# Performance work log

Hardware: AMD Instinct MI355X
Metric: run time of the kernel (lower is better)

The kernel has to match this reference:

```python
import jax, jax.numpy as jnp
import numpy as np

D_MODEL = 1024
NUM_HEADS = 16
HEAD_DIM = D_MODEL // NUM_HEADS


def setup_inputs() -> dict:
    key = jax.random.key(0)
    ks = jax.random.split(key, 11)
    N, S = 4, 2048
    s = 1.0 / np.sqrt(D_MODEL)
    return {
        "query": jax.random.normal(ks[0], (N, S, D_MODEL), jnp.float32),
        "key": jax.random.normal(ks[1], (N, S, D_MODEL), jnp.float32),
        "value": jax.random.normal(ks[2], (N, S, D_MODEL), jnp.float32),
        "Wq": jax.random.normal(ks[3], (D_MODEL, D_MODEL), jnp.float32) * s,
        "bq": jnp.zeros((D_MODEL,), jnp.float32),
        "Wk": jax.random.normal(ks[4], (D_MODEL, D_MODEL), jnp.float32) * s,
        "bk": jnp.zeros((D_MODEL,), jnp.float32),
        "Wv": jax.random.normal(ks[5], (D_MODEL, D_MODEL), jnp.float32) * s,
        "bv": jnp.zeros((D_MODEL,), jnp.float32),
        "Wo": jax.random.normal(ks[6], (D_MODEL, D_MODEL), jnp.float32) * s,
        "bo": jnp.zeros((D_MODEL,), jnp.float32),
    }


def reference(query, key, value, Wq, bq, Wk, bk, Wv, bv, Wo, bo):
    N, Q, _ = query.shape
    K = key.shape[1]
    # torch Linear: x @ W^T + b
    q = (query @ Wq.T + bq).reshape(N, Q, NUM_HEADS, HEAD_DIM)
    k = (key @ Wk.T + bk).reshape(N, K, NUM_HEADS, HEAD_DIM)
    v = (value @ Wv.T + bv).reshape(N, K, NUM_HEADS, HEAD_DIM)
    # NOTE: original module applies NO 1/sqrt(head_dim) scaling.
    scores = jnp.einsum('nqhd,nkhd->nhqk', q, k)
    attn = jax.nn.softmax(scores, axis=3)
    out = jnp.einsum('nhqk,nkhd->nqhd', attn, v).reshape(N, Q, D_MODEL)
    return out @ Wo.T + bo
```

## Files before the change

### kernel.cpp

```cpp
#include <hip/hip_runtime.h>
#include <stdint.h>

#define SEQ 2048
#define MROWS 8192
#define LOG2E 1.44269504f

typedef __attribute__((ext_vector_type(8))) _Float16 f16x8;
typedef __attribute__((ext_vector_type(2))) __fp16 fp16x2_t;
typedef __attribute__((ext_vector_type(8))) unsigned short ushort8;
typedef __attribute__((ext_vector_type(4))) unsigned short ushort4_t;
typedef __attribute__((ext_vector_type(4))) float f32x4;

__device__ __forceinline__ unsigned short f32_to_f16u(float f) {
  union { _Float16 h; unsigned short u; } v; v.h = (_Float16)f; return v.u;
}

__device__ __forceinline__ ushort8 pack8_rtz(float4 f0, float4 f1) {
  union { fp16x2_t h2[4]; ushort8 u8; } pk;
  pk.h2[0] = __builtin_amdgcn_cvt_pkrtz(f0.x, f0.y);
  pk.h2[1] = __builtin_amdgcn_cvt_pkrtz(f0.z, f0.w);
  pk.h2[2] = __builtin_amdgcn_cvt_pkrtz(f1.x, f1.y);
  pk.h2[3] = __builtin_amdgcn_cvt_pkrtz(f1.z, f1.w);
  return pk.u8;
}

__device__ __forceinline__ void gload16(const void* g, void* l) {
  __builtin_amdgcn_global_load_lds(
      (const __attribute__((address_space(1))) unsigned int*)g,
      (__attribute__((address_space(3))) unsigned int*)l, 16, 0, 0);
}

__global__ __launch_bounds__(256) void wconv_k(
    const float* __restrict__ Wq, const float* __restrict__ Wk,
    const float* __restrict__ Wv, const float* __restrict__ Wo,
    unsigned short* __restrict__ WF)
{
  const int plane = blockIdx.y;
  const float* __restrict__ s = (plane==0)? Wq : (plane==1)? Wk : (plane==2)? Wv : Wo;
  size_t off = ((size_t)blockIdx.x*256 + threadIdx.x) * 8;
  float4 f0 = *(const float4*)(s + off);
  float4 f1 = *(const float4*)(s + off + 4);
  *(ushort8*)&WF[(size_t)plane*1048576 + off] = pack8_rtz(f0, f1);
}

__global__ __launch_bounds__(256) void qkv_k(
    const float* __restrict__ Aq, const float* __restrict__ Ak, const float* __restrict__ Av,
    const unsigned short* __restrict__ WF,
    const float* __restrict__ bq, const float* __restrict__ bk, const float* __restrict__ bv,
    unsigned short* __restrict__ Qf, unsigned short* __restrict__ Kf, unsigned short* __restrict__ Vt)
{
  const int z = blockIdx.z;
  const float* __restrict__ A    = (z==0)? Aq : (z==1)? Ak : Av;
  const unsigned short* __restrict__ W = WF + (size_t)z*1048576;
  const float* __restrict__ bias = (z==0)? bq : (z==1)? bk : bv;

  __shared__ unsigned short Ah[128*32];
  __shared__ unsigned short Bh[128*32];

  const int tid  = threadIdx.x;
  const int lane = tid & 63;
  const int w    = tid >> 6;
  const int wm   = w >> 1, wn = w & 1;
  const int row0 = blockIdx.x * 128;
  const int col0 = blockIdx.y * 128;

  f32x4 acc[4][4] = {};

  for (int k0 = 0; k0 < 1024; k0 += 32) {
    __syncthreads();
    #pragma unroll
    for (int j=0;j<2;++j) {
      int r  = w*32 + j*16 + (lane>>2);
      int sl = (lane & 3) ^ ((r>>1)&3);
      gload16(W + (size_t)(col0 + r)*1024 + k0 + sl*8, &Bh[(w*32 + j*16)*32]);
    }
    #pragma unroll
    for (int i = 0; i < 2; ++i) {
      int c = tid + i*256;
      int r = c >> 2, slot = c & 3;
      int lidx = r*32 + ((slot ^ ((r >> 1) & 3))*8);
      const float* ap = A + (size_t)(row0 + r)*1024 + k0 + slot*8;
      float4 f0 = *(const float4*)ap;
      float4 f1 = *(const float4*)(ap + 4);
      *(ushort8*)&Ah[lidx] = pack8_rtz(f0, f1);
    }
    __syncthreads();

    f16x8 a_[4], b_[4];
    const int slotR = lane >> 4;
    #pragma unroll
    for (int m=0;m<4;++m) {
      int r = wm*64 + m*16 + (lane & 15);
      a_[m] = *(const f16x8*)&Ah[r*32 + ((slotR ^ ((r>>1)&3))*8)];
    }
    #pragma unroll
    for (int nn=0;nn<4;++nn) {
      int r = wn*64 + nn*16 + (lane & 15);
      b_[nn] = *(const f16x8*)&Bh[r*32 + ((slotR ^ ((r>>1)&3))*8)];
    }
    #pragma unroll
    for (int m=0;m<4;++m)
      #pragma unroll
      for (int nn=0;nn<4;++nn)
        acc[m][nn] = __builtin_amdgcn_mfma_f32_16x16x32_f16(a_[m], b_[nn], acc[m][nn],0,0,0);
  }

  #pragma unroll
  for (int m=0;m<4;++m) {
    #pragma unroll
    for (int nn=0;nn<4;++nn) {
      int gcol = col0 + wn*64 + nn*16 + (lane & 15);
      float bsv = bias[gcol];
      if (z == 2) {
        int rbase = row0 + wm*64 + m*16 + (lane>>4)*4;
        int nIdx = rbase >> 11, s0 = rbase & 2047;
        ushort4_t pk;
        #pragma unroll
        for (int r2=0;r2<4;++r2) pk[r2] = f32_to_f16u(acc[m][nn][r2] + bsv);
        *(ushort4_t*)&Vt[((size_t)(nIdx*1024 + gcol))*2048 + s0] = pk;
      } else {
        unsigned short* __restrict__ dst = (z==0)? Qf : Kf;
        const float qsc = (z==0)? LOG2E : 1.0f;
        #pragma unroll
        for (int r2=0;r2<4;++r2) {
          int grow = row0 + wm*64 + m*16 + (lane>>4)*4 + r2;
          dst[(size_t)grow*1024 + gcol] = f32_to_f16u((acc[m][nn][r2] + bsv) * qsc);
        }
      }
    }
  }
}

__global__ __launch_bounds__(256) void oproj_k(
    const unsigned short* __restrict__ AO, const unsigned short* __restrict__ W,
    const float* __restrict__ bias, float* __restrict__ out)
{
  __shared__ unsigned short Ah[128*32];
  __shared__ unsigned short Bh[128*32];

  const int tid  = threadIdx.x;
  const int lane = tid & 63;
  const int w    = tid >> 6;
  const int wm   = w >> 1, wn = w & 1;
  const int row0 = blockIdx.x * 128;
  const int col0 = blockIdx.y * 128;

  f32x4 acc[4][4] = {};

  for (int k0 = 0; k0 < 1024; k0 += 32) {
    __syncthreads();
    #pragma unroll
    for (int j=0;j<2;++j) {
      int r  = w*32 + j*16 + (lane>>2);
      int sl = (lane & 3) ^ ((r>>1)&3);
      gload16(AO + (size_t)(row0 + r)*1024 + k0 + sl*8, &Ah[(w*32 + j*16)*32]);
      gload16(W  + (size_t)(col0 + r)*1024 + k0 + sl*8, &Bh[(w*32 + j*16)*32]);
    }
    __syncthreads();

    f16x8 a_[4], b_[4];
    const int slotR = lane >> 4;
    #pragma unroll
    for (int m=0;m<4;++m) {
      int r = wm*64 + m*16 + (lane & 15);
      a_[m] = *(const f16x8*)&Ah[r*32 + ((slotR ^ ((r>>1)&3))*8)];
    }
    #pragma unroll
    for (int nn=0;nn<4;++nn) {
      int r = wn*64 + nn*16 + (lane & 15);
      b_[nn] = *(const f16x8*)&Bh[r*32 + ((slotR ^ ((r>>1)&3))*8)];
    }
    #pragma unroll
    for (int m=0;m<4;++m)
      #pragma unroll
      for (int nn=0;nn<4;++nn)
        acc[m][nn] = __builtin_amdgcn_mfma_f32_16x16x32_f16(a_[m], b_[nn], acc[m][nn],0,0,0);
  }

  #pragma unroll
  for (int m=0;m<4;++m)
    #pragma unroll
    for (int nn=0;nn<4;++nn) {
      int gcol = col0 + wn*64 + nn*16 + (lane & 15);
      float bsv = bias[gcol];
      #pragma unroll
      for (int r2=0;r2<4;++r2) {
        int grow = row0 + wm*64 + m*16 + (lane>>4)*4 + r2;
        out[(size_t)grow*1024 + gcol] = acc[m][nn][r2] + bsv;
      }
    }
}

__global__ __launch_bounds__(256) void attn_k(
  const unsigned short* __restrict__ Qf, const unsigned short* __restrict__ Kf,
  const unsigned short* __restrict__ Vt, unsigned short* __restrict__ AO)
{
  __shared__ unsigned short Ks[2][64*64];
  __shared__ unsigned short Vs[2][64*64];
  __shared__ unsigned short Ps[4][32*64];

  const int tid = threadIdx.x, lane = tid & 63, w = tid >> 6;
  const int q = lane & 15, g = lane >> 4;

  const int bid = blockIdx.x;
  const int swz = (bid & 7) * 128 + (bid >> 3);
  const int qt = swz & 15, nh = swz >> 4;
  const int n = nh >> 4, h = nh & 15;

  f16x8 qf[2][2];
  #pragma unroll
  for (int qm=0; qm<2; ++qm) {
    int qrow = n*SEQ + qt*128 + w*32 + qm*16 + q;
    #pragma unroll
    for (int ks=0; ks<2; ++ks)
      qf[qm][ks] = *(const f16x8*)&Qf[(size_t)qrow*1024 + h*64 + ks*32 + g*8];
  }

  f32x4 o[2][4] = {};
  float mrun[2] = {-1e30f,-1e30f}, lrun[2] = {0.f,0.f};

  const size_t kbase = (size_t)(n*SEQ)*1024 + h*64;
  const size_t vbase = ((size_t)(n*1024 + h*64))*SEQ;

  #pragma unroll
  for (int i=0;i<2;++i){
    int c = tid + i*256; int r = c>>3, sl = c&7;
    int lidx = r*64 + ((sl^(r&7))*8);
    *(ushort8*)&Ks[0][lidx] = *(const ushort8*)&Kf[kbase + (size_t)r*1024 + sl*8];
    *(ushort8*)&Vs[0][lidx] = *(const ushort8*)&Vt[vbase + (size_t)r*SEQ + sl*8];
  }
  __syncthreads();

  int cur = 0;
  for (int kt = 0; kt < 32; ++kt) {
    f32x4 s[2][4];
    #pragma unroll
    for (int qm=0;qm<2;++qm)
      #pragma unroll
      for (int nf=0; nf<4; ++nf) s[qm][nf] = f32x4{0.f,0.f,0.f,0.f};
    __builtin_amdgcn_s_setprio(1);
    #pragma unroll
    for (int nf=0; nf<4; ++nf) {
      int rr = nf*16 + q;
      #pragma unroll
      for (int ks=0; ks<2; ++ks) {
        f16x8 kb = *(const f16x8*)&Ks[cur][rr*64 + (((ks*4+g)^(q&7))*8)];
        s[0][nf] = __builtin_amdgcn_mfma_f32_16x16x32_f16(kb, qf[0][ks], s[0][nf],0,0,0);
        s[1][nf] = __builtin_amdgcn_mfma_f32_16x16x32_f16(kb, qf[1][ks], s[1][nf],0,0,0);
      }
    }
    __builtin_amdgcn_s_setprio(0);

    ushort8 kreg[2], vreg[2];
    if (kt < 31) {
      #pragma unroll
      for (int i=0;i<2;++i){
        int c = tid + i*256; int r = c>>3, sl = c&7;
        kreg[i] = *(const ushort8*)&Kf[kbase + (size_t)((kt+1)*64 + r)*1024 + sl*8];
        vreg[i] = *(const ushort8*)&Vt[vbase + (size_t)r*SEQ + (kt+1)*64 + sl*8];
      }
    }

    #pragma unroll
    for (int qm=0; qm<2; ++qm) {
      float ml = fmaxf(fmaxf(fmaxf(s[qm][0][0],s[qm][0][1]),fmaxf(s[qm][0][2],s[qm][0][3])),
                       fmaxf(fmaxf(s[qm][1][0],s[qm][1][1]),fmaxf(s[qm][1][2],s[qm][1][3])));
      float mh = fmaxf(fmaxf(fmaxf(s[qm][2][0],s[qm][2][1]),fmaxf(s[qm][2][2],s[qm][2][3])),
                       fmaxf(fmaxf(s[qm][3][0],s[qm][3][1]),fmaxf(s[qm][3][2],s[qm][3][3])));
      ml = fmaxf(ml, mh);
      if (!__all(ml <= mrun[qm] + 7.0f)) {
        float m1 = fmaxf(ml, __shfl_xor(ml, 16, 64));
        float m2 = fmaxf(m1, __shfl_xor(m1, 32, 64));
        float mn = fmaxf(mrun[qm], m2);
        float sc = __builtin_amdgcn_exp2f(mrun[qm] - mn);
        lrun[qm] *= sc;
        mrun[qm] = mn;
        #pragma unroll
        for (int df=0; df<4; ++df)
          #pragma unroll
          for (int r=0;r<4;++r) o[qm][df][r] *= sc;
      }
      float m0 = mrun[qm];
      float pvv[16]; float rsl = 0.f;
      #pragma unroll
      for (int nf=0; nf<4; ++nf)
        #pragma unroll
        for (int r=0;r<4;++r) {
          float p = __builtin_amdgcn_exp2f(s[qm][nf][r] - m0);
          pvv[nf*4+r] = p; rsl += p;
        }
      lrun[qm] += rsl;

      #pragma unroll
      for (int nf=0; nf<4; ++nf) {
        union { fp16x2_t h2[2]; ushort4_t u4; } pk;
        pk.h2[0] = __builtin_amdgcn_cvt_pkrtz(pvv[nf*4+0], pvv[nf*4+1]);
        pk.h2[1] = __builtin_amdgcn_cvt_pkrtz(pvv[nf*4+2], pvv[nf*4+3]);
        int gi = 2*nf + (g>>1);
        int idx = (qm*16+q)*64 + ((gi ^ (q&7))*8) + (g&1)*4;
        *(ushort4_t*)&Ps[w][idx] = pk.u4;
      }
    }

    #pragma unroll
    for (int s2=0; s2<2; ++s2) {
      int sl = 4*s2 + g;
      f16x8 pa0 = *(const f16x8*)&Ps[w][(q    )*64 + ((sl^(q&7))*8)];
      f16x8 pa1 = *(const f16x8*)&Ps[w][(16+q)*64 + ((sl^(q&7))*8)];
      __builtin_amdgcn_s_setprio(1);
      #pragma unroll
      for (int df=0; df<4; ++df) {
        f16x8 vb = *(const f16x8*)&Vs[cur][(df*16+q)*64 + ((sl^(q&7))*8)];
        o[0][df] = __builtin_amdgcn_mfma_f32_16x16x32_f16(vb, pa0, o[0][df],0,0,0);
        o[1][df] = __builtin_amdgcn_mfma_f32_16x16x32_f16(vb, pa1, o[1][df],0,0,0);
      }
      __builtin_amdgcn_s_setprio(0);
    }

    if (kt < 31) {
      #pragma unroll
      for (int i=0;i<2;++i){
        int c = tid + i*256; int r = c>>3, sl = c&7;
        int lidx = r*64 + ((sl^(r&7))*8);
        *(ushort8*)&Ks[cur^1][lidx] = kreg[i];
        *(ushort8*)&Vs[cur^1][lidx] = vreg[i];
      }
    }
    __syncthreads();
    cur ^= 1;
  }

  #pragma unroll
  for (int qm=0; qm<2; ++qm) {
    float rs = lrun[qm];
    rs += __shfl_xor(rs, 16, 64);
    rs += __shfl_xor(rs, 32, 64);
    float inv = 1.0f / rs;
    int qrow = n*SEQ + qt*128 + w*32 + qm*16 + q;
    #pragma unroll
    for (int df=0; df<4; ++df)
      #pragma unroll
      for (int r=0;r<4;++r)
        AO[(size_t)qrow*1024 + h*64 + df*16 + g*4 + r] = f32_to_f16u(o[qm][df][r] * inv);
  }
}

extern "C" void kernel_launch(void* const* d_in, const int* in_sizes, int n_in,
                              void* d_out, int out_size, void* d_ws, size_t ws_size,
                              hipStream_t stream)
{
  (void)in_sizes; (void)n_in; (void)out_size; (void)ws_size;
  const float* query = (const float*)d_in[0];
  const float* key   = (const float*)d_in[1];
  const float* value = (const float*)d_in[2];
  const float* Wq = (const float*)d_in[3];
  const float* bq = (const float*)d_in[4];
  const float* Wk = (const float*)d_in[5];
  const float* bk = (const float*)d_in[6];
  const float* Wv = (const float*)d_in[7];
  const float* bv = (const float*)d_in[8];
  const float* Wo = (const float*)d_in[9];
  const float* bo = (const float*)d_in[10];
  float* out = (float*)d_out;

  unsigned short* ws = (unsigned short*)d_ws;
  const size_t PLANE = (size_t)MROWS * 1024;
  unsigned short* Qf = ws;
  unsigned short* Kf = Qf + PLANE;
  unsigned short* Vt = Kf + PLANE;
  unsigned short* AO = Vt + PLANE;
  unsigned short* WF = AO + PLANE;

  dim3 bb(256);
  wconv_k<<<dim3(512,4), bb, 0, stream>>>(Wq, Wk, Wv, Wo, WF);
  qkv_k <<<dim3(64,8,3), bb, 0, stream>>>(query,key,value, WF, bq,bk,bv, Qf,Kf,Vt);
  attn_k<<<dim3(1024), bb, 0, stream>>>(Qf, Kf, Vt, AO);
  oproj_k<<<dim3(64,8), bb, 0, stream>>>(AO, WF + 3*1048576, bo, out);
}
```

Baseline: 221.6 us.

## Use direct global-to-LDS loads and keep P in registers for PV MFMA

K/V tiles for the next iteration are now issued as direct global-to-LDS async loads at the top of the loop. This replaces the register staging and the later LDS stores. The softmax probabilities are packed into f16x4 fragments and fed straight into 16x16x16 MFMAs, which removes the per-wave P shared-memory round trip. In exchange it uses the smaller-K MFMA variant with twice as many instructions. It also depends on gload16 completing before the barrier, and on the source-side XOR swizzle matching the read pattern.

```diff
diff --git a/kernel.cpp b/kernel.cpp
--- a/kernel.cpp
+++ b/kernel.cpp
@@ -6,6 +6,7 @@
 #define LOG2E 1.44269504f
 
 typedef __attribute__((ext_vector_type(8))) _Float16 f16x8;
+typedef __attribute__((ext_vector_type(4))) _Float16 f16x4;
 typedef __attribute__((ext_vector_type(2))) __fp16 fp16x2_t;
 typedef __attribute__((ext_vector_type(8))) unsigned short ushort8;
 typedef __attribute__((ext_vector_type(4))) unsigned short ushort4_t;
@@ -197,7 +198,6 @@
 {
   __shared__ unsigned short Ks[2][64*64];
   __shared__ unsigned short Vs[2][64*64];
-  __shared__ unsigned short Ps[4][32*64];
 
   const int tid = threadIdx.x, lane = tid & 63, w = tid >> 6;
   const int q = lane & 15, g = lane >> 4;
@@ -222,17 +222,28 @@
   const size_t kbase = (size_t)(n*SEQ)*1024 + h*64;
   const size_t vbase = ((size_t)(n*1024 + h*64))*SEQ;
 
-  #pragma unroll
-  for (int i=0;i<2;++i){
-    int c = tid + i*256; int r = c>>3, sl = c&7;
-    int lidx = r*64 + ((sl^(r&7))*8);
-    *(ushort8*)&Ks[0][lidx] = *(const ushort8*)&Kf[kbase + (size_t)r*1024 + sl*8];
-    *(ushort8*)&Vs[0][lidx] = *(const ushort8*)&Vt[vbase + (size_t)r*SEQ + sl*8];
+  const int srow = lane >> 3;
+  const int ssl  = (lane & 7) ^ srow;
+
+  #pragma unroll
+  for (int j=0;j<2;++j) {
+    int r = w*16 + j*8 + srow;
+    gload16(&Kf[kbase + (size_t)r*1024 + ssl*8], &Ks[0][(w*16+j*8)*64]);
+    gload16(&Vt[vbase + (size_t)r*SEQ  + ssl*8], &Vs[0][(w*16+j*8)*64]);
   }
   __syncthreads();
 
   int cur = 0;
   for (int kt = 0; kt < 32; ++kt) {
+    if (kt < 31) {
+      #pragma unroll
+      for (int j=0;j<2;++j) {
+        int r = w*16 + j*8 + srow;
+        gload16(&Kf[kbase + (size_t)((kt+1)*64 + r)*1024 + ssl*8], &Ks[cur^1][(w*16+j*8)*64]);
+        gload16(&Vt[vbase + (size_t)r*SEQ + (kt+1)*64 + ssl*8],    &Vs[cur^1][(w*16+j*8)*64]);
+      }
+    }
+
     f32x4 s[2][4];
     #pragma unroll
     for (int qm=0;qm<2;++qm)
@@ -251,16 +262,7 @@
     }
     __builtin_amdgcn_s_setprio(0);
 
-    ushort8 kreg[2], vreg[2];
-    if (kt < 31) {
-      #pragma unroll
-      for (int i=0;i<2;++i){
-        int c = tid + i*256; int r = c>>3, sl = c&7;
-        kreg[i] = *(const ushort8*)&Kf[kbase + (size_t)((kt+1)*64 + r)*1024 + sl*8];
-        vreg[i] = *(const ushort8*)&Vt[vbase + (size_t)r*SEQ + (kt+1)*64 + sl*8];
-      }
-    }
-
+    f16x4 pfrag[2][4];
     #pragma unroll
     for (int qm=0; qm<2; ++qm) {
       float ml = fmaxf(fmaxf(fmaxf(s[qm][0][0],s[qm][0][1]),fmaxf(s[qm][0][2],s[qm][0][3])),
@@ -281,51 +283,40 @@
           for (int r=0;r<4;++r) o[qm][df][r] *= sc;
       }
       float m0 = mrun[qm];
-      float pvv[16]; float rsl = 0.f;
-      #pragma unroll
-      for (int nf=0; nf<4; ++nf)
-        #pragma unroll
-        for (int r=0;r<4;++r) {
-          float p = __builtin_amdgcn_exp2f(s[qm][nf][r] - m0);
-          pvv[nf*4+r] = p; rsl += p;
-        }
+      float rsl = 0.f;
+      #pragma unroll
+      for (int nf=0; nf<4; ++nf) {
+        float p0 = __builtin_amdgcn_exp2f(s[qm][nf][0] - m0);
+        float p1 = __builtin_amdgcn_exp2f(s[qm][nf][1] - m0);
+        float p2 = __builtin_amdgcn_exp2f(s[qm][nf][2] - m0);
+        float p3 = __builtin_amdgcn_exp2f(s[qm][nf][3] - m0);
+        rsl += (p0 + p1) + (p2 + p3);
+        union { fp16x2_t h2[2]; f16x4 h4; } pk;
+        pk.h2[0] = __builtin_amdgcn_cvt_pkrtz(p0, p1);
+        pk.h2[1] = __builtin_amdgcn_cvt_pkrtz(p2, p3);
+        pfrag[qm][nf] = pk.h4;
+      }
       lrun[qm] += rsl;
-
+    }
+
+    #pragma unroll
+    for (int df=0; df<4; ++df) {
+      int row = df*16 + q;
+      f16x4 va[4];
       #pragma unroll
       for (int nf=0; nf<4; ++nf) {
-        union { fp16x2_t h2[2]; ushort4_t u4; } pk;
-        pk.h2[0] = __builtin_amdgcn_cvt_pkrtz(pvv[nf*4+0], pvv[nf*4+1]);
-        pk.h2[1] = __builtin_amdgcn_cvt_pkrtz(pvv[nf*4+2], pvv[nf*4+3]);
-        int gi = 2*nf + (g>>1);
-        int idx = (qm*16+q)*64 + ((gi ^ (q&7))*8) + (g&1)*4;
-        *(ushort4_t*)&Ps[w][idx] = pk.u4;
-      }
-    }
-
-    #pragma unroll
-    for (int s2=0; s2<2; ++s2) {
-      int sl = 4*s2 + g;
-      f16x8 pa0 = *(const f16x8*)&Ps[w][(q    )*64 + ((sl^(q&7))*8)];
-      f16x8 pa1 = *(const f16x8*)&Ps[w][(16+q)*64 + ((sl^(q&7))*8)];
+        int gran = 2*nf + (g>>1);
+        va[nf] = *(const f16x4*)&Vs[cur][row*64 + ((gran ^ (row&7))*8) + (g&1)*4];
+      }
       __builtin_amdgcn_s_setprio(1);
       #pragma unroll
-      for (int df=0; df<4; ++df) {
-        f16x8 vb = *(const f16x8*)&Vs[cur][(df*16+q)*64 + ((sl^(q&7))*8)];
-        o[0][df] = __builtin_amdgcn_mfma_f32_16x16x32_f16(vb, pa0, o[0][df],0,0,0);
-        o[1][df] = __builtin_amdgcn_mfma_f32_16x16x32_f16(vb, pa1, o[1][df],0,0,0);
+      for (int nf=0; nf<4; ++nf) {
+        o[0][df] = __builtin_amdgcn_mfma_f32_16x16x16f16(va[nf], pfrag[0][nf], o[0][df],0,0,0);
+        o[1][df] = __builtin_amdgcn_mfma_f32_16x16x16f16(va[nf], pfrag[1][nf], o[1][df],0,0,0);
       }
       __builtin_amdgcn_s_setprio(0);
     }
 
-    if (kt < 31) {
-      #pragma unroll
-      for (int i=0;i<2;++i){
-        int c = tid + i*256; int r = c>>3, sl = c&7;
-        int lidx = r*64 + ((sl^(r&7))*8);
-        *(ushort8*)&Ks[cur^1][lidx] = kreg[i];
-        *(ushort8*)&Vs[cur^1][lidx] = vreg[i];
-      }
-    }
     __syncthreads();
     cur ^= 1;
   }
```

Measured after the change: 242.0 us. 9.2% more time.

## Switch attention to 32x32x16 MFMA and keep P in registers via permlane32 swap

Applied to the files above, without the earlier changes.

Rewrites the attention inner loop to use 32x32x16 MFMA tiles instead of 16x16x32. The softmax probabilities are packed to fp16 and rearranged across lanes with v_permlane32_swap, so they feed the PV MFMA directly from registers. This removes the per-wave LDS buffer for P along with its writes and reads, and cuts the cross-lane reductions to a single shuffle. The output store is also vectorized to 4 halves. The cost is a more complex lane layout and reliance on the gfx950 permlane instruction.

```diff
diff --git a/kernel.cpp b/kernel.cpp
--- a/kernel.cpp
+++ b/kernel.cpp
@@ -10,9 +10,16 @@
 typedef __attribute__((ext_vector_type(8))) unsigned short ushort8;
 typedef __attribute__((ext_vector_type(4))) unsigned short ushort4_t;
 typedef __attribute__((ext_vector_type(4))) float f32x4;
+typedef __attribute__((ext_vector_type(16))) float f32x16;
 
 __device__ __forceinline__ unsigned short f32_to_f16u(float f) {
   union { _Float16 h; unsigned short u; } v; v.h = (_Float16)f; return v.u;
+}
+
+__device__ __forceinline__ unsigned int pk_u32(float a, float b) {
+  union { fp16x2_t h; unsigned int u; } v;
+  v.h = __builtin_amdgcn_cvt_pkrtz(a, b);
+  return v.u;
 }
 
 __device__ __forceinline__ ushort8 pack8_rtz(float4 f0, float4 f1) {
@@ -197,30 +204,28 @@
 {
   __shared__ unsigned short Ks[2][64*64];
   __shared__ unsigned short Vs[2][64*64];
-  __shared__ unsigned short Ps[4][32*64];
 
   const int tid = threadIdx.x, lane = tid & 63, w = tid >> 6;
-  const int q = lane & 15, g = lane >> 4;
+  const int q = lane & 31, h = lane >> 5;
 
   const int bid = blockIdx.x;
   const int swz = (bid & 7) * 128 + (bid >> 3);
   const int qt = swz & 15, nh = swz >> 4;
-  const int n = nh >> 4, h = nh & 15;
-
-  f16x8 qf[2][2];
-  #pragma unroll
-  for (int qm=0; qm<2; ++qm) {
-    int qrow = n*SEQ + qt*128 + w*32 + qm*16 + q;
-    #pragma unroll
-    for (int ks=0; ks<2; ++ks)
-      qf[qm][ks] = *(const f16x8*)&Qf[(size_t)qrow*1024 + h*64 + ks*32 + g*8];
-  }
-
-  f32x4 o[2][4] = {};
-  float mrun[2] = {-1e30f,-1e30f}, lrun[2] = {0.f,0.f};
-
-  const size_t kbase = (size_t)(n*SEQ)*1024 + h*64;
-  const size_t vbase = ((size_t)(n*1024 + h*64))*SEQ;
+  const int n = nh >> 4, hh = nh & 15;
+
+  f16x8 qf[4];
+  {
+    int qrow = n*SEQ + qt*128 + w*32 + q;
+    #pragma unroll
+    for (int t=0;t<4;++t)
+      qf[t] = *(const f16x8*)&Qf[(size_t)qrow*1024 + hh*64 + t*16 + h*8];
+  }
+
+  f32x16 o[2] = {};
+  float mrun = -1e30f, lrun = 0.f;
+
+  const size_t kbase = (size_t)(n*SEQ)*1024 + hh*64;
+  const size_t vbase = ((size_t)(n*1024 + hh*64))*SEQ;
 
   #pragma unroll
   for (int i=0;i<2;++i){
@@ -233,24 +238,6 @@
 
   int cur = 0;
   for (int kt = 0; kt < 32; ++kt) {
-    f32x4 s[2][4];
-    #pragma unroll
-    for (int qm=0;qm<2;++qm)
-      #pragma unroll
-      for (int nf=0; nf<4; ++nf) s[qm][nf] = f32x4{0.f,0.f,0.f,0.f};
-    __builtin_amdgcn_s_setprio(1);
-    #pragma unroll
-    for (int nf=0; nf<4; ++nf) {
-      int rr = nf*16 + q;
-      #pragma unroll
-      for (int ks=0; ks<2; ++ks) {
-        f16x8 kb = *(const f16x8*)&Ks[cur][rr*64 + (((ks*4+g)^(q&7))*8)];
-        s[0][nf] = __builtin_amdgcn_mfma_f32_16x16x32_f16(kb, qf[0][ks], s[0][nf],0,0,0);
-        s[1][nf] = __builtin_amdgcn_mfma_f32_16x16x32_f16(kb, qf[1][ks], s[1][nf],0,0,0);
-      }
-    }
-    __builtin_amdgcn_s_setprio(0);
-
     ushort8 kreg[2], vreg[2];
     if (kt < 31) {
       #pragma unroll
@@ -261,59 +248,76 @@
       }
     }
 
-    #pragma unroll
-    for (int qm=0; qm<2; ++qm) {
-      float ml = fmaxf(fmaxf(fmaxf(s[qm][0][0],s[qm][0][1]),fmaxf(s[qm][0][2],s[qm][0][3])),
-                       fmaxf(fmaxf(s[qm][1][0],s[qm][1][1]),fmaxf(s[qm][1][2],s[qm][1][3])));
-      float mh = fmaxf(fmaxf(fmaxf(s[qm][2][0],s[qm][2][1]),fmaxf(s[qm][2][2],s[qm][2][3])),
-                       fmaxf(fmaxf(s[qm][3][0],s[qm][3][1]),fmaxf(s[qm][3][2],s[qm][3][3])));
-      ml = fmaxf(ml, mh);
-      if (!__all(ml <= mrun[qm] + 7.0f)) {
-        float m1 = fmaxf(ml, __shfl_xor(ml, 16, 64));
-        float m2 = fmaxf(m1, __shfl_xor(m1, 32, 64));
-        float mn = fmaxf(mrun[qm], m2);
-        float sc = __builtin_amdgcn_exp2f(mrun[qm] - mn);
-        lrun[qm] *= sc;
-        mrun[qm] = mn;
+    f32x16 s[2] = {};
+    __builtin_amdgcn_s_setprio(1);
+    #pragma unroll
+    for (int t=0; t<4; ++t) {
+      int gr = ((2*t+h) ^ (q&7))*8;
+      f16x8 k0 = *(const f16x8*)&Ks[cur][(q     )*64 + gr];
+      f16x8 k1 = *(const f16x8*)&Ks[cur][(32 + q)*64 + gr];
+      s[0] = __builtin_amdgcn_mfma_f32_32x32x16_f16(k0, qf[t], s[0],0,0,0);
+      s[1] = __builtin_amdgcn_mfma_f32_32x32x16_f16(k1, qf[t], s[1],0,0,0);
+    }
+    __builtin_amdgcn_s_setprio(0);
+
+    float m01 = fmaxf(fmaxf(s[0][0], s[0][1]), fmaxf(s[0][2], s[0][3]));
+    float m02 = fmaxf(fmaxf(s[0][4], s[0][5]), fmaxf(s[0][6], s[0][7]));
+    float m03 = fmaxf(fmaxf(s[0][8], s[0][9]), fmaxf(s[0][10], s[0][11]));
+    float m04 = fmaxf(fmaxf(s[0][12], s[0][13]), fmaxf(s[0][14], s[0][15]));
+    float m11 = fmaxf(fmaxf(s[1][0], s[1][1]), fmaxf(s[1][2], s[1][3]));
+    float m12 = fmaxf(fmaxf(s[1][4], s[1][5]), fmaxf(s[1][6], s[1][7]));
+    float m13 = fmaxf(fmaxf(s[1][8], s[1][9]), fmaxf(s[1][10], s[1][11]));
+    float m14 = fmaxf(fmaxf(s[1][12], s[1][13]), fmaxf(s[1][14], s[1][15]));
+    float ml = fmaxf(fmaxf(fmaxf(m01,m02), fmaxf(m03,m04)),
+                     fmaxf(fmaxf(m11,m12), fmaxf(m13,m14)));
+    if (!__all(ml <= mrun + 7.0f)) {
+      float m2 = fmaxf(ml, __shfl_xor(ml, 32, 64));
+      float mn = fmaxf(mrun, m2);
+      float sc = __builtin_amdgcn_exp2f(mrun - mn);
+      lrun *= sc;
+      mrun = mn;
+      #pragma unroll
+      for (int dd=0; dd<2; ++dd)
         #pragma unroll
-        for (int df=0; df<4; ++df)
-          #pragma unroll
-          for (int r=0;r<4;++r) o[qm][df][r] *= sc;
-      }
-      float m0 = mrun[qm];
-      float pvv[16]; float rsl = 0.f;
-      #pragma unroll
-      for (int nf=0; nf<4; ++nf)
+        for (int r=0;r<16;++r) o[dd][r] *= sc;
+    }
+    {
+      float m0 = mrun;
+      float rsl = 0.f;
+      #pragma unroll
+      for (int st=0; st<2; ++st)
         #pragma unroll
-        for (int r=0;r<4;++r) {
-          float p = __builtin_amdgcn_exp2f(s[qm][nf][r] - m0);
-          pvv[nf*4+r] = p; rsl += p;
+        for (int r=0;r<16;++r) {
+          float p = __builtin_amdgcn_exp2f(s[st][r] - m0);
+          s[st][r] = p; rsl += p;
         }
-      lrun[qm] += rsl;
-
-      #pragma unroll
-      for (int nf=0; nf<4; ++nf) {
-        union { fp16x2_t h2[2]; ushort4_t u4; } pk;
-        pk.h2[0] = __builtin_amdgcn_cvt_pkrtz(pvv[nf*4+0], pvv[nf*4+1]);
-        pk.h2[1] = __builtin_amdgcn_cvt_pkrtz(pvv[nf*4+2], pvv[nf*4+3]);
-        int gi = 2*nf + (g>>1);
-        int idx = (qm*16+q)*64 + ((gi ^ (q&7))*8) + (g&1)*4;
-        *(ushort4_t*)&Ps[w][idx] = pk.u4;
-      }
-    }
-
-    #pragma unroll
-    for (int s2=0; s2<2; ++s2) {
-      int sl = 4*s2 + g;
-      f16x8 pa0 = *(const f16x8*)&Ps[w][(q    )*64 + ((sl^(q&7))*8)];
-      f16x8 pa1 = *(const f16x8*)&Ps[w][(16+q)*64 + ((sl^(q&7))*8)];
+      lrun += rsl;
+    }
+
+    f16x8 pf[4];
+    #pragma unroll
+    for (int st=0; st<2; ++st)
+      #pragma unroll
+      for (int s_t=0; s_t<2; ++s_t) {
+        unsigned int a0 = pk_u32(s[st][8*s_t+0], s[st][8*s_t+1]);
+        unsigned int a1 = pk_u32(s[st][8*s_t+2], s[st][8*s_t+3]);
+        unsigned int b0 = pk_u32(s[st][8*s_t+4], s[st][8*s_t+5]);
+        unsigned int b1 = pk_u32(s[st][8*s_t+6], s[st][8*s_t+7]);
+        asm("v_permlane32_swap_b32 %0, %1" : "+v"(a0), "+v"(b0));
+        asm("v_permlane32_swap_b32 %0, %1" : "+v"(a1), "+v"(b1));
+        union { unsigned int u[4]; f16x8 v; } pkk;
+        pkk.u[0] = a0; pkk.u[1] = a1; pkk.u[2] = b0; pkk.u[3] = b1;
+        pf[st*2 + s_t] = pkk.v;
+      }
+
+    #pragma unroll
+    for (int sg=0; sg<4; ++sg) {
+      int gr = ((2*sg+h) ^ (q&7))*8;
+      f16x8 v0 = *(const f16x8*)&Vs[cur][(q     )*64 + gr];
+      f16x8 v1 = *(const f16x8*)&Vs[cur][(32 + q)*64 + gr];
       __builtin_amdgcn_s_setprio(1);
-      #pragma unroll
-      for (int df=0; df<4; ++df) {
-        f16x8 vb = *(const f16x8*)&Vs[cur][(df*16+q)*64 + ((sl^(q&7))*8)];
-        o[0][df] = __builtin_amdgcn_mfma_f32_16x16x32_f16(vb, pa0, o[0][df],0,0,0);
-        o[1][df] = __builtin_amdgcn_mfma_f32_16x16x32_f16(vb, pa1, o[1][df],0,0,0);
-      }
+      o[0] = __builtin_amdgcn_mfma_f32_32x32x16_f16(v0, pf[sg], o[0],0,0,0);
+      o[1] = __builtin_amdgcn_mfma_f32_32x32x16_f16(v1, pf[sg], o[1],0,0,0);
       __builtin_amdgcn_s_setprio(0);
     }
 
@@ -330,19 +334,19 @@
     cur ^= 1;
   }
 
+  float rs = lrun + __shfl_xor(lrun, 32, 64);
+  float inv = 1.0f / rs;
+  int qrow = n*SEQ + qt*128 + w*32 + q;
   #pragma unroll
-  for (int qm=0; qm<2; ++qm) {
-    float rs = lrun[qm];
-    rs += __shfl_xor(rs, 16, 64);
-    rs += __shfl_xor(rs, 32, 64);
-    float inv = 1.0f / rs;
-    int qrow = n*SEQ + qt*128 + w*32 + qm*16 + q;
-    #pragma unroll
-    for (int df=0; df<4; ++df)
-      #pragma unroll
-      for (int r=0;r<4;++r)
-        AO[(size_t)qrow*1024 + h*64 + df*16 + g*4 + r] = f32_to_f16u(o[qm][df][r] * inv);
-  }
+  for (int dd=0; dd<2; ++dd)
+    #pragma unroll
+    for (int rq=0; rq<4; ++rq) {
+      union { fp16x2_t h2[2]; ushort4_t u4; } pk4;
+      pk4.h2[0] = __builtin_amdgcn_cvt_pkrtz(o[dd][4*rq+0]*inv, o[dd][4*rq+1]*inv);
+      pk4.h2[1] = __builtin_amdgcn_cvt_pkrtz(o[dd][4*rq+2]*inv, o[dd][4*rq+3]*inv);
+      int d0 = dd*32 + 8*rq + 4*h;
+      *(ushort4_t*)&AO[(size_t)qrow*1024 + hh*64 + d0] = pk4.u4;
+    }
 }
 
 extern "C" void kernel_launch(void* const* d_in, const int* in_sizes, int n_in,
```

Result: no change. 222.6 us (+0.5%).
